# Kernel optimization log

Hardware: AMD Instinct MI355X
Metric: run time of the kernel (lower is better)

## Reference

```python
import jax, jax.numpy as jnp
import numpy as np

RANK = 16
SCALE = 0.05  # keep I + J well-conditioned


def setup_inputs() -> dict:
    key = jax.random.key(0)
    k1, k2 = jax.random.split(key)
    B, N_E = 262144, 128
    occ_so = jax.random.normal(k1, (B, N_E), dtype=jnp.float32)
    W = jax.random.normal(k2, (N_E, RANK * RANK), dtype=jnp.float32) * SCALE
    b = jnp.zeros((RANK * RANK,), dtype=jnp.float32)
    return {"occ_so": occ_so, "W": W, "b": b}


def reference(occ_so, W, b):
    # Parametrizer head: (..., n_e) -> (..., r*r)
    r = RANK
    batch_shape = occ_so.shape[:-1]
    j = occ_so @ W + b                       # (B, r*r)
    j = j.reshape(batch_shape + (r, r))      # (B, r, r)
    I = jnp.eye(r, dtype=j.dtype)
    j_sign, j_logabs = jnp.linalg.slogdet(I + j)
    return (j_sign, j_logabs)
```

## Files before the change

kernel.cpp:

```cpp
#include <hip/hip_runtime.h>
#include <cstdint>

typedef __attribute__((ext_vector_type(8))) short short8;
typedef __attribute__((ext_vector_type(4))) float f32x4;
typedef __attribute__((ext_vector_type(2))) float f32x2;

#define NE 128
#define RR 256
#define MT 64
#define JST 260

__device__ __forceinline__ float u2f(unsigned u) { return __builtin_bit_cast(float, u); }
__device__ __forceinline__ unsigned f2u(float f) { return __builtin_bit_cast(unsigned, f); }
__device__ __forceinline__ unsigned short f2bf(float x) {
  unsigned u = f2u(x);
  unsigned r = (u + 0x7FFFu + ((u >> 16) & 1u)) >> 16;
  return (unsigned short)r;
}
__device__ __forceinline__ float bf2f(unsigned short h) {
  return u2f(((unsigned)h) << 16);
}
__device__ __forceinline__ float bperm_f(int byteidx, float v) {
  return __builtin_bit_cast(float,
      __builtin_amdgcn_ds_bpermute(byteidx, __builtin_bit_cast(int, v)));
}
template<int CTRL>
__device__ __forceinline__ unsigned dpp_maxu(unsigned k) {
  unsigned o = (unsigned)__builtin_amdgcn_update_dpp(0, (int)k, CTRL, 0xF, 0xF, true);
  return o > k ? o : k;
}

__device__ __forceinline__ void split3(float x, unsigned short& a,
                                       unsigned short& b, unsigned short& c) {
  unsigned short h1 = f2bf(x);
  float r1 = x - bf2f(h1);
  unsigned short h2 = f2bf(r1);
  float r2 = r1 - bf2f(h2);
  a = h1; b = h2; c = f2bf(r2);
}

__global__ __launch_bounds__(256)
void wsplit3_kernel(const float* __restrict__ W,
                    unsigned short* __restrict__ wh,
                    unsigned short* __restrict__ wm,
                    unsigned short* __restrict__ wl) {
  int t = blockIdx.x * 256 + threadIdx.x;
  int k = t >> 8, col = t & 255;
  unsigned short h1, h2, h3;
  split3(W[t], h1, h2, h3);
  int kt = k >> 5, klo = k & 31;
  int lane = ((klo >> 3) << 4) | (col & 15);
  int u = klo & 7;
  int ct = col >> 4;
  int e = ((kt * 16 + ct) * 64 + lane) * 8 + u;
  wh[e] = h1; wm[e] = h2; wl[e] = h3;
}

__global__ __launch_bounds__(256, 2)
void jastrow_mfma(const float* __restrict__ occ,
                  const unsigned short* __restrict__ wh,
                  const unsigned short* __restrict__ wm,
                  const unsigned short* __restrict__ wl,
                  const float* __restrict__ bias,
                  float* __restrict__ out, int B) {
  __shared__ __align__(16) char smem[MT * JST * 4];
  float* occS = (float*)smem;
  float* jbuf = (float*)smem;

  const int tid  = threadIdx.x;
  const int lane = tid & 63;
  const int wv   = tid >> 6;
  const int wr   = wv >> 1;
  const int wc   = wv & 1;
  const int l15  = lane & 15;
  const int lh   = lane >> 4;
  const long long b0 = (long long)blockIdx.x * MT;

  {
    const float* src = occ + b0 * NE;
    #pragma unroll
    for (int p = 0; p < 8; p++) {
      int flat = (tid + p * 256) * 4;
      int row = flat >> 7, e = flat & 127;
      f32x4 v = *(const f32x4*)(src + flat);
      *(f32x4*)(occS + row * 132 + e) = v;
    }
  }
  __syncthreads();

  short8 Ah[2][4], Am[2][4], Al[2][4];
  #pragma unroll
  for (int rt = 0; rt < 2; rt++) {
    #pragma unroll
    for (int kt = 0; kt < 4; kt++) {
      const float* p = occS + (wr * 32 + rt * 16 + l15) * 132 + kt * 32 + lh * 8;
      f32x4 v0 = *(const f32x4*)p;
      f32x4 v1 = *(const f32x4*)(p + 4);
      float xs[8] = {v0[0], v0[1], v0[2], v0[3], v1[0], v1[1], v1[2], v1[3]};
      #pragma unroll
      for (int u = 0; u < 8; u++) {
        unsigned short h1, h2, h3;
        split3(xs[u], h1, h2, h3);
        Ah[rt][kt][u] = (short)h1;
        Am[rt][kt][u] = (short)h2;
        Al[rt][kt][u] = (short)h3;
      }
    }
  }
  __syncthreads();

  f32x4 acc[2][8];
  #pragma unroll
  for (int ct = 0; ct < 8; ct++) {
    float bv = bias[(wc * 8 + ct) * 16 + l15];
    f32x4 a; a[0] = bv; a[1] = bv; a[2] = bv; a[3] = bv;
    acc[0][ct] = a; acc[1][ct] = a;
  }
  #pragma unroll
  for (int kt = 0; kt < 4; kt++) {
    #pragma unroll
    for (int ct = 0; ct < 8; ct++) {
      const int ctg = wc * 8 + ct;
      int fo = ((kt * 16 + ctg) * 64 + lane) * 8;
      short8 bh = *(const short8*)(wh + fo);
      short8 bm = *(const short8*)(wm + fo);
      short8 bl = *(const short8*)(wl + fo);
      #pragma unroll
      for (int rt = 0; rt < 2; rt++) {
        f32x4 c = acc[rt][ct];
        c = __builtin_amdgcn_mfma_f32_16x16x32_bf16(Ah[rt][kt], bh, c, 0, 0, 0);
        c = __builtin_amdgcn_mfma_f32_16x16x32_bf16(Ah[rt][kt], bm, c, 0, 0, 0);
        c = __builtin_amdgcn_mfma_f32_16x16x32_bf16(Am[rt][kt], bh, c, 0, 0, 0);
        c = __builtin_amdgcn_mfma_f32_16x16x32_bf16(Am[rt][kt], bm, c, 0, 0, 0);
        c = __builtin_amdgcn_mfma_f32_16x16x32_bf16(Ah[rt][kt], bl, c, 0, 0, 0);
        c = __builtin_amdgcn_mfma_f32_16x16x32_bf16(Al[rt][kt], bh, c, 0, 0, 0);
        acc[rt][ct] = c;
      }
    }
  }

  #pragma unroll
  for (int ct = 0; ct < 8; ct++) {
    const int ctg = wc * 8 + ct;
    #pragma unroll
    for (int rt = 0; rt < 2; rt++) {
      #pragma unroll
      for (int i = 0; i < 4; i++) {
        int m = wr * 32 + rt * 16 + lh * 4 + i;
        jbuf[m * JST + ctg * 16 + l15] = acc[rt][ct][i];
      }
    }
  }
  __syncthreads();

  const int l4 = lane & 3;
  const int g  = lane >> 2;
  const int gm = wv * 16 + g;
  #define XW(i, j) (xp[i][(j) >> 1][(j) & 1])

  f32x2 xp[4][8];
  #pragma unroll
  for (int i = 0; i < 4; i++) {
    #pragma unroll
    for (int c4 = 0; c4 < 4; c4++) {
      f32x4 v = *(const f32x4*)&jbuf[gm * JST + (l4 + 4 * i) * 16 + c4 * 4];
      f32x2 t0; t0[0] = v[0]; t0[1] = v[1];
      f32x2 t1; t1[0] = v[2]; t1[1] = v[3];
      xp[i][c4 * 2]     = t0;
      xp[i][c4 * 2 + 1] = t1;
    }
  }
  #pragma unroll
  for (int i = 0; i < 4; i++) {
    xp[i][2*i][0]     += (l4 == 0) ? 1.0f : 0.0f;
    xp[i][2*i][1]     += (l4 == 1) ? 1.0f : 0.0f;
    xp[i][2*i + 1][0] += (l4 == 2) ? 1.0f : 0.0f;
    xp[i][2*i + 1][1] += (l4 == 3) ? 1.0f : 0.0f;
  }

  unsigned used = 0u;
  int par = 0;
  int esum = 0;
  float prodm = 1.0f;
  const int lbase = (lane & 60) << 2;
  #pragma unroll
  for (int k = 0; k < 16; k++) {
    float xk[4];
    unsigned kmax = 0u;
    #pragma unroll
    for (int i = 0; i < 4; i++) {
      xk[i] = XW(i, k);
      bool act = ((used >> (l4 + 4 * i)) & 1u) == 0u;
      unsigned ab = f2u(fabsf(xk[i]));
      unsigned code = (unsigned)(15 - 4 * i) - (unsigned)l4;
      unsigned key = act ? ((ab & 0xFFFFFFE0u) | 0x10u | code) : 0u;
      kmax = key > kmax ? key : kmax;
    }
    kmax = dpp_maxu<0xB1>(kmax);
    kmax = dpp_maxu<0x4E>(kmax);
    const int p = 15 - (int)(kmax & 0xFu);
    const bool pb0 = (p & 4) != 0;
    const bool pb1 = (p & 8) != 0;
    const int bidx = lbase | ((p & 3) << 2);

    float s01 = pb0 ? XW(1, k) : XW(0, k);
    float s23 = pb0 ? XW(3, k) : XW(2, k);
    float piv = bperm_f(bidx, pb1 ? s23 : s01);

    int e; float mant = frexpf(piv, &e);
    prodm *= mant; esum += e;
    par ^= __popc(used & (0xFFFFFFFFu << (p + 1))) & 1;
    used |= 1u << p;

    float rp = (piv != 0.0f) ? (1.0f / piv) : 0.0f;

    f32x2 mf[4];
    #pragma unroll
    for (int i = 0; i < 4; i++) {
      bool act = ((used >> (l4 + 4 * i)) & 1u) == 0u;
      float f = act ? xk[i] * rp : 0.0f;
      mf[i][0] = -f; mf[i][1] = -f;
    }
    #pragma unroll
    for (int jp = (k + 1) >> 1; jp < 8; jp++) {
      float a01 = pb0 ? XW(1, 2 * jp) : XW(0, 2 * jp);
      float a23 = pb0 ? XW(3, 2 * jp) : XW(2, 2 * jp);
      float t0 = bperm_f(bidx, pb1 ? a23 : a01);
      float b01 = pb0 ? XW(1, 2 * jp + 1) : XW(0, 2 * jp + 1);
      float b23 = pb0 ? XW(3, 2 * jp + 1) : XW(2, 2 * jp + 1);
      float t1 = bperm_f(bidx, pb1 ? b23 : b01);
      f32x2 tp; tp[0] = t0; tp[1] = t1;
      #pragma unroll
      for (int i = 0; i < 4; i++)
        xp[i][jp] = __builtin_elementwise_fma(tp, mf[i], xp[i][jp]);
    }
  }
  if (l4 == 0) {
    float la = (__log2f(fabsf(prodm)) + (float)esum) * 0.6931471805599453f;
    int neg = (prodm < 0.0f) ? 1 : 0;
    float sg = (prodm == 0.0f) ? 0.0f : (((neg ^ par) != 0) ? -1.0f : 1.0f);
    long long b = b0 + gm;
    out[b] = sg;
    out[(long long)B + b] = la;
  }
  #undef XW
}

extern "C" void kernel_launch(void* const* d_in, const int* in_sizes, int n_in,
                              void* d_out, int out_size, void* d_ws, size_t ws_size,
                              hipStream_t stream) {
  const float* occ  = (const float*)d_in[0];
  const float* Wg   = (const float*)d_in[1];
  const float* bias = (const float*)d_in[2];
  float* out = (float*)d_out;
  const int B = in_sizes[0] / NE;
  unsigned short* wh = (unsigned short*)d_ws;
  unsigned short* wm = wh + NE * RR;
  unsigned short* wl = wm + NE * RR;

  hipLaunchKernelGGL(wsplit3_kernel, dim3(NE * RR / 256), dim3(256), 0, stream,
                     Wg, wh, wm, wl);
  hipLaunchKernelGGL(jastrow_mfma, dim3(B / MT), dim3(256), 0, stream,
                     occ, wh, wm, wl, bias, out, B);
}
```

Measured before the change: 143.9 us.

## Halve block tile to 32 rows and split GEMM columns across four waves

Reduces the batch tile from 64 to 32 rows, with each of four waves computing a 32x64 slice of the output columns instead of a 32x128 slice. The bf16 split fragments of occ are now computed per k-tile inside the GEMM loop rather than held for all k up front, and the accumulator array is halved, which cuts register pressure and shared memory per block so more blocks can reside per CU. In exchange every wave redundantly splits the full A tile, weight fragments are loaded twice as often per row, and only two of four waves do the slogdet elimination, leaving half the block idle in that phase.

Result: slower. 159.0 us (+10.5%).

```diff
diff --git a/kernel.cpp b/kernel.cpp
--- a/kernel.cpp
+++ b/kernel.cpp
@@ -7,7 +7,7 @@
 
 #define NE 128
 #define RR 256
-#define MT 64
+#define MT 32
 #define JST 260
 
 __device__ __forceinline__ float u2f(unsigned u) { return __builtin_bit_cast(float, u); }
@@ -56,7 +56,7 @@
   wh[e] = h1; wm[e] = h2; wl[e] = h3;
 }
 
-__global__ __launch_bounds__(256, 2)
+__global__ __launch_bounds__(256)
 void jastrow_mfma(const float* __restrict__ occ,
                   const unsigned short* __restrict__ wh,
                   const unsigned short* __restrict__ wm,
@@ -70,8 +70,6 @@
   const int tid  = threadIdx.x;
   const int lane = tid & 63;
   const int wv   = tid >> 6;
-  const int wr   = wv >> 1;
-  const int wc   = wv & 1;
   const int l15  = lane & 15;
   const int lh   = lane >> 4;
   const long long b0 = (long long)blockIdx.x * MT;
@@ -79,7 +77,7 @@
   {
     const float* src = occ + b0 * NE;
     #pragma unroll
-    for (int p = 0; p < 8; p++) {
+    for (int p = 0; p < 4; p++) {
       int flat = (tid + p * 256) * 4;
       int row = flat >> 7, e = flat & 127;
       f32x4 v = *(const f32x4*)(src + flat);
@@ -88,12 +86,19 @@
   }
   __syncthreads();
 
-  short8 Ah[2][4], Am[2][4], Al[2][4];
-  #pragma unroll
-  for (int rt = 0; rt < 2; rt++) {
-    #pragma unroll
-    for (int kt = 0; kt < 4; kt++) {
-      const float* p = occS + (wr * 32 + rt * 16 + l15) * 132 + kt * 32 + lh * 8;
+  f32x4 acc[2][4];
+  #pragma unroll
+  for (int ct = 0; ct < 4; ct++) {
+    float bv = bias[(wv * 4 + ct) * 16 + l15];
+    f32x4 a; a[0] = bv; a[1] = bv; a[2] = bv; a[3] = bv;
+    acc[0][ct] = a; acc[1][ct] = a;
+  }
+  #pragma unroll
+  for (int kt = 0; kt < 4; kt++) {
+    short8 Ah[2], Am[2], Al[2];
+    #pragma unroll
+    for (int rt = 0; rt < 2; rt++) {
+      const float* p = occS + (rt * 16 + l15) * 132 + kt * 32 + lh * 8;
       f32x4 v0 = *(const f32x4*)p;
       f32x4 v1 = *(const f32x4*)(p + 4);
       float xs[8] = {v0[0], v0[1], v0[2], v0[3], v1[0], v1[1], v1[2], v1[3]};
@@ -101,26 +106,14 @@
       for (int u = 0; u < 8; u++) {
         unsigned short h1, h2, h3;
         split3(xs[u], h1, h2, h3);
-        Ah[rt][kt][u] = (short)h1;
-        Am[rt][kt][u] = (short)h2;
-        Al[rt][kt][u] = (short)h3;
+        Ah[rt][u] = (short)h1;
+        Am[rt][u] = (short)h2;
+        Al[rt][u] = (short)h3;
       }
     }
-  }
-  __syncthreads();
-
-  f32x4 acc[2][8];
-  #pragma unroll
-  for (int ct = 0; ct < 8; ct++) {
-    float bv = bias[(wc * 8 + ct) * 16 + l15];
-    f32x4 a; a[0] = bv; a[1] = bv; a[2] = bv; a[3] = bv;
-    acc[0][ct] = a; acc[1][ct] = a;
-  }
-  #pragma unroll
-  for (int kt = 0; kt < 4; kt++) {
-    #pragma unroll
-    for (int ct = 0; ct < 8; ct++) {
-      const int ctg = wc * 8 + ct;
+    #pragma unroll
+    for (int ct = 0; ct < 4; ct++) {
+      const int ctg = wv * 4 + ct;
       int fo = ((kt * 16 + ctg) * 64 + lane) * 8;
       short8 bh = *(const short8*)(wh + fo);
       short8 bm = *(const short8*)(wm + fo);
@@ -128,30 +121,33 @@
       #pragma unroll
       for (int rt = 0; rt < 2; rt++) {
         f32x4 c = acc[rt][ct];
-        c = __builtin_amdgcn_mfma_f32_16x16x32_bf16(Ah[rt][kt], bh, c, 0, 0, 0);
-        c = __builtin_amdgcn_mfma_f32_16x16x32_bf16(Ah[rt][kt], bm, c, 0, 0, 0);
-        c = __builtin_amdgcn_mfma_f32_16x16x32_bf16(Am[rt][kt], bh, c, 0, 0, 0);
-        c = __builtin_amdgcn_mfma_f32_16x16x32_bf16(Am[rt][kt], bm, c, 0, 0, 0);
-        c = __builtin_amdgcn_mfma_f32_16x16x32_bf16(Ah[rt][kt], bl, c, 0, 0, 0);
-        c = __builtin_amdgcn_mfma_f32_16x16x32_bf16(Al[rt][kt], bh, c, 0, 0, 0);
+        c = __builtin_amdgcn_mfma_f32_16x16x32_bf16(Ah[rt], bh, c, 0, 0, 0);
+        c = __builtin_amdgcn_mfma_f32_16x16x32_bf16(Ah[rt], bm, c, 0, 0, 0);
+        c = __builtin_amdgcn_mfma_f32_16x16x32_bf16(Am[rt], bh, c, 0, 0, 0);
+        c = __builtin_amdgcn_mfma_f32_16x16x32_bf16(Am[rt], bm, c, 0, 0, 0);
+        c = __builtin_amdgcn_mfma_f32_16x16x32_bf16(Ah[rt], bl, c, 0, 0, 0);
+        c = __builtin_amdgcn_mfma_f32_16x16x32_bf16(Al[rt], bh, c, 0, 0, 0);
         acc[rt][ct] = c;
       }
     }
   }
-
-  #pragma unroll
-  for (int ct = 0; ct < 8; ct++) {
-    const int ctg = wc * 8 + ct;
+  __syncthreads();
+
+  #pragma unroll
+  for (int ct = 0; ct < 4; ct++) {
+    const int ctg = wv * 4 + ct;
     #pragma unroll
     for (int rt = 0; rt < 2; rt++) {
       #pragma unroll
       for (int i = 0; i < 4; i++) {
-        int m = wr * 32 + rt * 16 + lh * 4 + i;
+        int m = rt * 16 + lh * 4 + i;
         jbuf[m * JST + ctg * 16 + l15] = acc[rt][ct][i];
       }
     }
   }
   __syncthreads();
+
+  if (wv >= 2) return;
 
   const int l4 = lane & 3;
   const int g  = lane >> 2;
```
